# Performance work log

Hardware: AMD Instinct MI355X
Metric: run time of the kernel (lower is better)

Reference implementation:

```python
import jax, jax.numpy as jnp
import numpy as np

B, H, W, DIM = 4, 128, 128, 64
HEADS, DH, DR = 8, 64, 16
INNER = HEADS * DH  # 512
HID3 = 3 * DR       # 48, wavelet-MLP in_channels
HIDX = 2 * HID3     # 96, wavelet-MLP hidden


def _conv(x, w, stride=1, pad=0, groups=1):
    return jax.lax.conv_general_dilated(
        x, w, (stride, stride), [(pad, pad), (pad, pad)],
        dimension_numbers=('NCHW', 'OIHW', 'NCHW'), feature_group_count=groups)


def _gelu(x):
    return jax.nn.gelu(x, approximate=False)  # torch nn.GELU default (erf)


def _haar_kernel(C):
    h = np.array([[1., 1.], [1., 1.]]) / 2.
    g = np.array([[1., -1.], [1., -1.]]) / 2.
    ht = np.array([[1., 1.], [-1., -1.]]) / 2.
    gt = np.array([[1., -1.], [-1., 1.]]) / 2.
    k = np.stack([h, g, ht, gt])[:, None]          # [4,1,2,2]
    return jnp.asarray(np.tile(k, (C, 1, 1, 1)), jnp.float32)  # [4C,1,2,2], torch repeat layout


def _l2norm(x):
    return x / jnp.maximum(jnp.linalg.norm(x, axis=-1, keepdims=True), 1e-12)


def _spatial(x, dw, pw, gamma):  # SpitialUnit, x NHWC
    t = x.transpose(0, 3, 1, 2)
    C = t.shape[1]
    y = _conv(t, dw, pad=1, groups=C)
    y = _conv(_gelu(y), pw)
    return (t + gamma * y).transpose(0, 2, 3, 1)


def _fourier(x, al_pw, al_dw, ah_pw, ah_dw, ph_pw, ph_scale):  # FourierUnit, x NHWC
    t = x.transpose(0, 3, 1, 2)
    Bc, C, Hc, Wc = t.shape
    X = jnp.fft.rfft2(t, norm='ortho')
    amp, phase = jnp.abs(X), jnp.angle(X)
    Hf, Wf = amp.shape[-2], amp.shape[-1]
    yy = jnp.linspace(0., 1., Hf)[:, None]
    xx = jnp.linspace(0., 1., Wf)[None, :]
    rr = jnp.sqrt(yy ** 2 + xx ** 2)
    low = jax.nn.sigmoid((0.25 - rr) * 20.0)
    high = 1.0 - low
    a_lo = _conv(_gelu(_conv(amp * low[None, None], al_pw)), al_dw, pad=1, groups=C)
    a_hi = _conv(_gelu(_conv(amp * high[None, None], ah_pw)), ah_dw, pad=1, groups=C)
    amp_out = a_lo + a_hi
    phase_out = phase + ph_scale * _conv(phase, ph_pw)
    Y = jax.lax.complex(amp_out * jnp.cos(phase_out), amp_out * jnp.sin(phase_out))
    out = jnp.fft.irfft2(Y, s=(Hc, Wc), norm='ortho')
    return out.transpose(0, 2, 3, 1)


def _wavelet(x, bn_gamma, bn_beta, mlp_in, mlp_dw, mlp_out, res_scale):  # WaveletUnit, x NHWC (H,W even)
    t = x.transpose(0, 3, 1, 2)
    Bc, C, Hc, Wc = t.shape
    y = _conv(t, _haar_kernel(C), stride=2, groups=C)           # [B,4C,H/2,W/2]
    LL, LH, HL, HH = jnp.split(y, 4, axis=1)                    # torch chunk layout
    high = jnp.concatenate([LH, HL, HH], axis=1)                # [B,3C,H/2,W/2]
    # BatchNorm2d in eval mode: running_mean=0, running_var=1, eps=1e-5
    n = high * (bn_gamma / jnp.sqrt(1.0 + 1e-5))[None, :, None, None] + bn_beta[None, :, None, None]
    m = _conv(n, mlp_in)
    m = _gelu(_conv(m, mlp_dw, pad=1, groups=m.shape[1]))
    m = _conv(m, mlp_out)
    high_enh = high + res_scale * m
    x1, x2, x3 = jnp.split(high_enh, 3, axis=1)
    # IWT: out[..., 2i+p, 2j+q] = [LL, x1; x2, x3][p,q]
    arr = jnp.stack([jnp.stack([LL, x1], -1), jnp.stack([x2, x3], -1)], axis=-2)  # [B,C,h,w,p,q]
    Hh, Wh = LL.shape[-2], LL.shape[-1]
    out = arr.transpose(0, 1, 2, 4, 3, 5).reshape(Bc, C, Hh * 2, Wh * 2)
    return out.transpose(0, 2, 3, 1)


def reference(x_in, Wq, Wk, Wv, Wr, We, qs_dw, qs_pw, qs_gamma,
              al_pw, al_dw, ah_pw, ah_dw, ph_pw, ph_scale,
              bn_gamma, bn_beta, mlp_in, mlp_dw, mlp_out, res_scale,
              rescale, Wproj, bproj):
    b, h, w, c = x_in.shape
    hw = h * w
    heads = rescale.shape[0]
    dh = Wq.shape[1] // heads
    dr = Wr.shape[1]
    x = x_in.reshape(b, hw, c)
    q_inp, k_inp, v_inp = x @ Wq, x @ Wk, x @ Wv
    q_dim = (q_inp @ Wr).reshape(b, h, w, dr)
    k_dim = (k_inp @ Wr).reshape(b, h, w, dr)
    v_dim = (v_inp @ Wr).reshape(b, h, w, dr)
    q_mix = _spatial(q_dim, qs_dw, qs_pw, qs_gamma)
    k_mix = _fourier(k_dim, al_pw, al_dw, ah_pw, ah_dw, ph_pw, ph_scale)
    v_mix = _wavelet(v_dim, bn_gamma, bn_beta, mlp_in, mlp_dw, mlp_out, res_scale)
    q_new = q_mix.reshape(b, hw, dr) @ We
    k_new = k_mix.reshape(b, hw, dr) @ We
    v_new = v_mix.reshape(b, hw, dr) @ We

    def pack(t):  # -> [b, heads, dh, hw]
        return t.reshape(b, hw, heads, dh).transpose(0, 2, 3, 1)

    q, k, v = pack(q_new), pack(k_new), pack(v_new)
    q, k = _l2norm(q), _l2norm(k)                       # normalize over hw
    attn = jnp.einsum('bhdn,bhen->bhde', k, q)          # channel attention [b,H,dh,dh]
    attn = jax.nn.softmax(attn * rescale[None], axis=-1)
    o = jnp.einsum('bhde,bhen->bhdn', attn, v)          # [b,H,dh,hw]
    o = o.transpose(0, 3, 1, 2).reshape(b, hw, heads * dh)
    return (o @ Wproj + bproj).reshape(b, h, w, c)


def setup_inputs() -> dict:
    key = jax.random.key(0)
    ks = jax.random.split(key, 20)

    def nrm(k, shape, s=0.02):
        return jax.random.normal(k, shape, jnp.float32) * s

    return {
        'x_in': jax.random.normal(ks[0], (B, H, W, DIM), jnp.float32),
        'Wq': nrm(ks[1], (DIM, INNER)), 'Wk': nrm(ks[2], (DIM, INNER)), 'Wv': nrm(ks[3], (DIM, INNER)),
        'Wr': nrm(ks[4], (INNER, DR)), 'We': nrm(ks[5], (DR, INNER)),
        'qs_dw': nrm(ks[6], (DR, 1, 3, 3)), 'qs_pw': nrm(ks[7], (DR, DR, 1, 1)),
        'qs_gamma': jnp.zeros((1, DR, 1, 1), jnp.float32),
        'al_pw': nrm(ks[8], (DR, DR, 1, 1)), 'al_dw': nrm(ks[9], (DR, 1, 3, 3)),
        'ah_pw': nrm(ks[10], (DR, DR, 1, 1)), 'ah_dw': nrm(ks[11], (DR, 1, 3, 3)),
        'ph_pw': nrm(ks[12], (DR, DR, 1, 1)), 'ph_scale': jnp.asarray(0.01, jnp.float32),
        'bn_gamma': jnp.ones((HID3,), jnp.float32), 'bn_beta': jnp.zeros((HID3,), jnp.float32),
        'mlp_in': nrm(ks[13], (HIDX, HID3, 1, 1)), 'mlp_dw': nrm(ks[14], (HIDX, 1, 3, 3)),
        'mlp_out': nrm(ks[15], (HID3, HIDX, 1, 1)), 'res_scale': jnp.ones((1,), jnp.float32),
        'rescale': jnp.ones((HEADS, 1, 1), jnp.float32),
        'Wproj': nrm(ks[16], (INNER, DIM)), 'bproj': jnp.zeros((DIM,), jnp.float32),
    }
```

## Files before the change

kernel.cpp:

```cpp
#include <hip/hip_runtime.h>
#include <hip/hip_bf16.h>
#include <math.h>

#define HW 16384

__device__ __forceinline__ float LD(const void* p, long i, int bf){
  return bf ? __bfloat162float(((const __hip_bfloat16*)p)[i]) : ((const float*)p)[i];
}
__device__ __forceinline__ float geluf(float x){ return 0.5f*x*(1.0f + erff(x*0.70710678118654752f)); }
__device__ __forceinline__ int rev7(int i){ return (int)(__brev((unsigned)i)>>25); }

__device__ __forceinline__ void fft128(float* Ar, float* Ai, const float* ct, const float* st,
                                       int lane, float dir){
  #pragma unroll
  for(int len=2; len<=128; len<<=1){
    int half=len>>1;
    int pos = lane & (half-1);
    int i1 = ((lane & ~(half-1))<<1) | pos;
    int i2 = i1 + half;
    int tw = pos * (128/len);
    float wr = ct[tw], wi = dir*st[tw];
    float xr=Ar[i2], xi=Ai[i2];
    float tr = xr*wr - xi*wi;
    float ti = xr*wi + xi*wr;
    float ur=Ar[i1], ui=Ai[i1];
    Ar[i1]=ur+tr; Ai[i1]=ui+ti;
    Ar[i2]=ur-tr; Ai[i2]=ui-ti;
  }
}

#define MAKE_TWP(ct,st) { int tt=threadIdx.x; if(tt<128){ float ang=6.283185307179586f*(float)tt/128.f; float s_,c_; sincosf(ang,&s_,&c_); (ct)[tt]=c_; (st)[tt]=s_; } }

#define OFF_M    0
#define OFF_G    3072
#define OFF_MB   6144
#define OFF_FLAG 10240
#define OFF_QDIM 16384
#define OFF_KDIM (16384 + 1048576)
#define OFF_VDIM (16384 + 2*1048576)
#define OFF_QMIX (16384 + 3*1048576)
#define OFF_KMIX (16384 + 4*1048576)
#define OFF_S    (16384 + 5*1048576)
#define FSZ 532480

__global__ void k_head(const void* Wq, const void* Wk, const void* Wv,
                       const void* Wr, const void* bng, float* ws){
  __shared__ float wr[8192];
  __shared__ float part[256];
  int blk=blockIdx.x, t=threadIdx.x;
  if(blk==48){
    for(int i=3072+t;i<10240;i+=256) ws[i]=0.f;
    if(t==0){
      float v = ((const float*)bng)[0];
      ((int*)ws)[OFF_FLAG] = (v==1.0f) ? 0 : 1;
    }
    return;
  }
  int bf = (((const float*)bng)[0]==1.0f) ? 0 : 1;
  int mat=blk>>4, seg=blk&15;
  const void* Wsrc = mat==0 ? Wq : (mat==1 ? Wk : Wv);
  for(int i=t;i<8192;i+=256) wr[i]=LD(Wr,i,bf);
  __syncthreads();
  int o=t&63, jseg=t>>6;
  int c=seg*4+(o>>4), r=o&15;
  float acc=0.f;
  for(int j=jseg*128;j<jseg*128+128;j++) acc += LD(Wsrc,(long)c*512+j,bf)*wr[j*16+r];
  part[jseg*64+o]=acc;
  __syncthreads();
  if(t<64){
    float s=part[t]+part[64+t]+part[128+t]+part[192+t];
    int cc=seg*4+(t>>4), rr=t&15;
    ws[cc*48 + mat*16 + rr]=s;
  }
}

__global__ void k_dims(const void* x, const float* ws,
                       float* qd, float* kd, float* vd, const int* flg){
  int bf=*flg;
  __shared__ __align__(16) float ms[3072];
  __shared__ __align__(16) float xs[64*130];
  int t=threadIdx.x;
  int b = blockIdx.x>>7;
  int pix0 = (blockIdx.x&127)<<7;
  for(int i=t;i<3072;i+=256) ms[i]=ws[i];
  long base = ((long)b*HW + pix0)*64;
  if(!bf){
    const float4* xp = (const float4*)((const float*)x + base);
    for(int e=t;e<2048;e+=256){
      int px=e>>4, c4=(e&15)<<2;
      float4 v = xp[e];
      xs[(c4  )*130+px]=v.x; xs[(c4+1)*130+px]=v.y;
      xs[(c4+2)*130+px]=v.z; xs[(c4+3)*130+px]=v.w;
    }
  } else {
    const uint4* xp = (const uint4*)((const __hip_bfloat16*)x + base);
    for(int e=t;e<1024;e+=256){
// ... 129 lines not shown
    float* wiT=smem;
    float* vds=smem+4800;
    float* ns =smem+6848;
    float* gsm=smem+8416;
    float* bsm=smem+8464;
    int blk3=blk-512;
    int b = blk3>>7;
    int hpbase = (blk3&127)<<5;
    int i0 = hpbase>>6, j0 = hpbase&63;
    for(int i=t;i<4608;i+=256){ int ch=i/48, cc=i-ch*48; wiT[cc*100+ch]=LD(win,i,bf); }
    if(t<48){ gsm[t]=LD(bng,t,bf)*(1.f/sqrtf(1.f+1e-5f)); bsm[t]=LD(bnb,t,bf); }
    long rb0 = ((long)(b*128 + 2*i0)*128 + 2*j0)*16;
    {
      const float4* v4a=(const float4*)(vd+rb0);
      const float4* v4b=(const float4*)(vd+rb0+2048);
      ((float4*)vds)[t] = v4a[t];
      ((float4*)(vds+1024))[t] = v4b[t];
    }
    __syncthreads();
    for(int o=t;o<1536;o+=256){
      int p=o/48, cc=o-p*48;
      int m=cc+16, c=m>>2, f=m&3;
      float a =vds[(2*p)*16+c],      bv=vds[(2*p+1)*16+c];
      float cv=vds[1024+(2*p)*16+c], dvv=vds[1024+(2*p+1)*16+c];
      float v;
      if(f==0)      v=(a+bv+cv+dvv);
      else if(f==1) v=(a-bv+cv-dvv);
      else if(f==2) v=(a+bv-cv-dvv);
      else          v=(a-bv-cv+dvv);
      ns[p*49+cc] = v*0.5f*gsm[cc]+bsm[cc];
    }
    __syncthreads();
    int px=t>>3, chg=t&7;
    int ch0=chg*12;
    float4 a0={0,0,0,0}, a1={0,0,0,0}, a2={0,0,0,0};
    #pragma unroll 4
    for(int cc=0;cc<48;cc++){
      float nsv = ns[px*49+cc];
      const float4* wp = (const float4*)&wiT[cc*100+ch0];
      float4 w0=wp[0], w1=wp[1], w2=wp[2];
      a0.x+=nsv*w0.x; a0.y+=nsv*w0.y; a0.z+=nsv*w0.z; a0.w+=nsv*w0.w;
      a1.x+=nsv*w1.x; a1.y+=nsv*w1.y; a1.z+=nsv*w1.z; a1.w+=nsv*w1.w;
      a2.x+=nsv*w2.x; a2.y+=nsv*w2.y; a2.z+=nsv*w2.z; a2.w+=nsv*w2.w;
    }
    long ob = ((long)b*4096 + hpbase + px)*96 + ch0;
    float4* mp=(float4*)(m96+ob);
    mp[0]=a0; mp[1]=a1; mp[2]=a2;
  }
}

__global__ void k_fft_col(const float* Rre, const float* Rim,
                          float* glo, float* ghi, float* pho,
                          const void* alpw, const void* ahpw,
                          const void* phpw, const void* phs, const int* flg){
  __shared__ float sre[2080], sim[2080];
  __shared__ float og[2080], oh[2080], op[2080];
  __shared__ float Ar[512], Ai[512];
  __shared__ float ct[128], st[128];
  __shared__ float wl[256], wh[256], wp[256];
  int t=threadIdx.x;
  int bf=*flg;
  int b = blockIdx.x/65, v = blockIdx.x%65;
  MAKE_TWP(ct,st);
  wl[t]=LD(alpw,t,bf); wh[t]=LD(ahpw,t,bf); wp[t]=LD(phpw,t,bf);
  long ibase = ((long)b*128)*1040 + v*16;
  for(int e=t;e<2048;e+=256){
    int y=e>>4, c=e&15;
    sre[c*130+y]=Rre[ibase + (long)y*1040 + c];
    sim[c*130+y]=Rim[ibase + (long)y*1040 + c];
  }
  __syncthreads();
  int w=t>>6, l=t&63, wb=w<<7;
  const float inv=1.f/128.f;
  for(int c=w; c<16; c+=4){
    int sb=c*130;
    float x0r=sre[sb+l], x0i=sim[sb+l], x1r=sre[sb+64+l], x1i=sim[sb+64+l];
    int r0=rev7(l), r1=rev7(64+l);
    Ar[wb+r0]=x0r; Ai[wb+r0]=x0i;
    Ar[wb+r1]=x1r; Ai[wb+r1]=x1i;
    fft128(Ar+wb, Ai+wb, ct, st, l, -1.f);
    float re0=Ar[wb+l]*inv, im0=Ai[wb+l]*inv;
    float re1=Ar[wb+64+l]*inv, im1=Ai[wb+64+l]*inv;
    sre[sb+l]=sqrtf(re0*re0+im0*im0); sim[sb+l]=atan2f(im0,re0);
    sre[sb+64+l]=sqrtf(re1*re1+im1*im1); sim[sb+64+l]=atan2f(im1,re1);
  }
  __syncthreads();
  {
    int u = t&127, half = t>>7;
    float yy=(float)u/127.f, xx=(float)v/64.f;
    float rr=sqrtf(yy*yy+xx*xx);
    float lo = 1.f/(1.f+expf((rr-0.25f)*20.f));
    float hi = 1.f-lo;
    float av[16], pv[16];
    for(int ch=0;ch<16;ch++){ av[ch]=sre[ch*130+u]; pv[ch]=sim[ch*130+u]; }
    float pscale = LD(phs,0,bf);
    for(int c=half*8;c<half*8+8;c++){
      float al=0.f, ah=0.f, pp=0.f;
      for(int ch=0;ch<16;ch++){
        float a=av[ch];
        al += wl[c*16+ch]*(a*lo);
        ah += wh[c*16+ch]*(a*hi);
        pp += wp[c*16+ch]*pv[ch];
      }
      og[c*130+u]=geluf(al); oh[c*130+u]=geluf(ah); op[c*130+u]=pv[c]+pscale*pp;
    }
  }
  __syncthreads();
  long obase = ((long)b*128)*1040 + v*16;
  for(int e=t;e<2048;e+=256){
    int u=e>>4, c=e&15;
    long o = obase + (long)u*1040 + c;
    glo[o]=og[c*130+u]; ghi[o]=oh[c*130+u]; pho[o]=op[c*130+u];
  }
}

__global__ void k_four_dw(const float* glo, const float* ghi, const float* pho,
                          float* Yre, float* Yim,
                          const void* aldw, const void* ahdw, const int* flg){
  int bf=*flg;
  __shared__ float wl[144], wh[144];
  int t=threadIdx.x;
  if(t<144){wl[t]=LD(aldw,t,bf); wh[t]=LD(ahdw,t,bf);}
  __syncthreads();
  long o = (long)blockIdx.x*256+t;
  int c=(int)(o&15); long r=o>>4; int v=(int)(r%65); long r2=r/65; int u=(int)(r2&127); int b=(int)(r2>>7);
  float acc=0.f;
  for(int dp=0;dp<3;dp++){
    int uu=u-1+dp; if(uu<0||uu>=128) continue;
    for(int dq=0;dq<3;dq++){
      int vv=v-1+dq; if(vv<0||vv>=65) continue;
      long idx=(((long)(b*128+uu))*65+vv)*16+c;
      acc += wl[c*9+dp*3+dq]*glo[idx] + wh[c*9+dp*3+dq]*ghi[idx];
    }
  }
  float pvv = pho[o];
  float s_,c_; sincosf(pvv,&s_,&c_);
  Yre[o]=acc*c_; Yim[o]=acc*s_;
}

__global__ void k_ifft_col(const float* Yre, const float* Yim, float* Zre, float* Zim){
  __shared__ float sre[2080], sim[2080];
  __shared__ float Ar[512], Ai[512];
  __shared__ float ct[128], st[128];
  int t=threadIdx.x;
  int b = blockIdx.x/65, v = blockIdx.x%65;
  MAKE_TWP(ct,st);
  long ibase = ((long)b*128)*1040 + v*16;
  for(int e=t;e<2048;e+=256){
    int u=e>>4, c=e&15;
    sre[c*130+u]=Yre[ibase + (long)u*1040 + c];
    sim[c*130+u]=Yim[ibase + (long)u*1040 + c];
  }
  __syncthreads();
  int w=t>>6, l=t&63, wb=w<<7;
  for(int c=w; c<16; c+=4){
    int sb=c*130;
    float x0r=sre[sb+l], x0i=sim[sb+l], x1r=sre[sb+64+l], x1i=sim[sb+64+l];
    int r0=rev7(l), r1=rev7(64+l);
    Ar[wb+r0]=x0r; Ai[wb+r0]=x0i;
    Ar[wb+r1]=x1r; Ai[wb+r1]=x1i;
    fft128(Ar+wb, Ai+wb, ct, st, l, +1.f);
    sre[sb+l]=Ar[wb+l]; sim[sb+l]=Ai[wb+l];
    sre[sb+64+l]=Ar[wb+64+l]; sim[sb+64+l]=Ai[wb+64+l];
  }
  __syncthreads();
  for(int e=t;e<2048;e+=256){
    int y=e>>4, c=e&15;
    Zre[ibase + (long)y*1040 + c]=sre[c*130+y];
    Zim[ibase + (long)y*1040 + c]=sim[c*130+y];
  }
}

__global__ void k_mix2(const float* Zre, const float* Zim, const float* qm,
                       const float* m96, float* g96, const void* wdw_,
                       float* G, const int* flg){
  __shared__ float smem[9664];
  int blk=blockIdx.x, t=threadIdx.x;
  if(blk<256){
    float* szre=smem; float* szim=smem+2112; float* oslab=smem+4224;
    float* Ar=smem+8384; float* Ai=smem+8896; float* ct=smem+9408; float* st=smem+9536;
    int b = blk>>6, y0 = (blk&63)<<1;
    MAKE_TWP(ct,st);
    long ibase = ((long)(b*128+y0))*1040;
    for(int e=t;e<2080;e+=256){
      int yl=e/1040, rem=e%1040, v=rem>>4, c=rem&15;
      szre[yl*1056 + c*66 + v]=Zre[ibase+e];
      szim[yl*1056 + c*66 + v]=Zim[ibase+e];
    }
    __syncthreads();
    int w=t>>6, l=t&63, wb=w<<7;
    const float inv=1.f/128.f;
    for(int li=w; li<32; li+=4){
      int yl=li>>4, c=li&15;
      int sb = yl*1056 + c*66;
      float zr0 = szre[sb+l];
      float zi0 = (l==0)?0.f:szim[sb+l];
      float zr1, zi1;
      if(l==0){ zr1=szre[sb+64]; zi1=0.f; }
      else    { zr1=szre[sb+64-l]; zi1=-szim[sb+64-l]; }
      int r0=rev7(l), r1=rev7(64+l);
      Ar[wb+r0]=zr0; Ai[wb+r0]=zi0;
      Ar[wb+r1]=zr1; Ai[wb+r1]=zi1;
      fft128(Ar+wb, Ai+wb, ct, st, l, +1.f);
      int ob = yl*2080 + c*130;
      oslab[ob+l]=Ar[wb+l]*inv;
      oslab[ob+64+l]=Ar[wb+64+l]*inv;
    }
    __syncthreads();
    float* qs = smem;
    long qbase = ((long)(b*128+y0))*2048;
    for(int e=t;e<4096;e+=256) qs[e]=qm[qbase+e];
    __syncthreads();
    int r=t>>4, s=t&15;
    float akq=0.f, akk=0.f, aqq=0.f;
    for(int p=0;p<256;p++){
      int yl=p>>7, x=p&127;
      float kr = oslab[yl*2080 + r*130 + x];
      float ks_ = oslab[yl*2080 + s*130 + x];
      float qr = qs[p*16+r];
      float qsv= qs[p*16+s];
      akq += kr*qsv;
      akk += kr*ks_;
      aqq += qr*qsv;
    }
    float* Gb=G + b*768;
    atomicAdd(&Gb[t], akq);
    atomicAdd(&Gb[256+t], akk);
    atomicAdd(&Gb[512+t], aqq);
  } else {
    int bf=*flg;
    float* wdw=smem;
    for(int i=t;i<864;i+=256) wdw[i]=LD(wdw_,i,bf);
    __syncthreads();
    int o = (blk-256)*256+t;
    int ch = o%96; int r = o/96; int px = r&4095; int b = r>>12;
    int i = px>>6, j = px&63;
    long mb = (long)b*393216;
    float acc=0.f;
    for(int dp=0;dp<3;dp++){ int ii=i-1+dp; if(ii<0||ii>=64) continue;
      for(int dq=0;dq<3;dq++){ int jj=j-1+dq; if(jj<0||jj>=64) continue;
        acc += wdw[ch*9+dp*3+dq]*m96[mb + (long)(ii*64+jj)*96 + ch]; } }
    g96[o]=geluf(acc);
  }
}

__global__ void k_attn(const float* G, float* Mb, const void* We,
                       const void* Wproj, const void* resc, const int* flg){
  int bf=*flg;
  __shared__ float wes[16*64];
  __shared__ float gkq[256], gkk[256], gqq[256];
  __shared__ float ukq[64*16], ukk[64*16], uqq[64*16];
  __shared__ float nk[64], nq[64];
  __shared__ float A[64*64];
  __shared__ float T[64*16];
  __shared__ float wpj[64*64];
  int b=blockIdx.x>>3, h=blockIdx.x&7;
  int t=threadIdx.x;
  for(int i=t;i<1024;i+=256){ int rr=i>>6, e=i&63; wes[rr*64+e]=LD(We, (long)rr*512 + h*64 + e, bf); }
  gkq[t]=G[b*768+t]; gkk[t]=G[b*768+256+t]; gqq[t]=G[b*768+512+t];
  for(int i=t;i<4096;i+=256){ int d=i>>6, c=i&63; wpj[i]=LD(Wproj,(long)(h*64+d)*64+c,bf); }
  __syncthreads();
  for(int i=t;i<1024;i+=256){
    int d=i>>4, s=i&15;
    float a1=0.f,a2=0.f,a3=0.f;
    for(int rr=0;rr<16;rr++){ float wv=wes[rr*64+d]; a1+=wv*gkq[rr*16+s]; a2+=wv*gkk[rr*16+s]; a3+=wv*gqq[rr*16+s]; }
    ukq[i]=a1; ukk[i]=a2; uqq[i]=a3;
  }
  __syncthreads();
  if(t<64){ float a=0.f; for(int s=0;s<16;s++) a+=ukk[t*16+s]*wes[s*64+t]; nk[t]=fmaxf(sqrtf(a),1e-12f); }
  else if(t<128){ int e=t-64; float a=0.f; for(int s=0;s<16;s++) a+=uqq[e*16+s]*wes[s*64+e]; nq[e]=fmaxf(sqrtf(a),1e-12f); }
  __syncthreads();
  float rsc=LD(resc,h,bf);
  for(int i=t;i<4096;i+=256){
    int d=i>>6, e=i&63;
    float a=0.f; for(int s=0;s<16;s++) a+=ukq[d*16+s]*wes[s*64+e];
    A[i]=a/(nk[d]*nq[e])*rsc;
  }
  __syncthreads();
  if(t<64){
    int d=t; float m=-1e30f;
    for(int e=0;e<64;e++) m=fmaxf(m,A[d*64+e]);
    float sum=0.f;
    for(int e=0;e<64;e++){ float ev=expf(A[d*64+e]-m); A[d*64+e]=ev; sum+=ev; }
    float inv=1.f/sum;
    for(int e=0;e<64;e++) A[d*64+e]*=inv;
  }
  __syncthreads();
  for(int i=t;i<1024;i+=256){
    int d=i>>4, s=i&15;
    float a=0.f; for(int e=0;e<64;e++) a+=A[d*64+e]*wes[s*64+e];
    T[i]=a;
  }
  __syncthreads();
  for(int i=t;i<1024;i+=256){
    int s=i>>6, c=i&63;
    float a=0.f; for(int d=0;d<64;d++) a+=T[d*16+s]*wpj[d*64+c];
    atomicAdd(&Mb[b*1024 + s*64 + c], a);
  }
}

__global__ void k_epi2(const float* g96, const float* vd, const float* Mb_,
                       const void* wout_, const void* rs_, const void* bproj,
                       void* out, const int* flg){
  int bf=*flg;
  __shared__ __align__(16) float sg[32*104];
  __shared__ __align__(16) float swt[48*100];
  __shared__ __align__(16) float smb[1024];
  __shared__ float sbias[64];
  int t=threadIdx.x;
  int b = blockIdx.x>>7;
  int rem = blockIdx.x&127;
  int gi = rem>>1;
  int gj0 = (rem&1)<<5;

  long gb = ((long)b*4096 + gi*64 + gj0)*96;
  for(int e=t;e<3072;e+=256){ int px=e/96, ch=e-px*96; sg[px*104+ch]=g96[gb+e]; }
  for(int e=t;e<4608;e+=256){ int cc=e/96, ch=e-cc*96; swt[cc*100+ch]=LD(wout_, e, bf); }
  for(int i=t;i<1024;i+=256) smb[i]=Mb_[b*1024+i];
  if(t<64) sbias[t]=LD(bproj,t,bf);
  __syncthreads();

  int tpx=t>>4, tcc=t&15;
  int px0=tpx<<1, cc0=tcc*3;
  float a00=0.f,a01=0.f,a02=0.f,a10=0.f,a11=0.f,a12=0.f;
  const float4* g4=(const float4*)sg;
  const float4* w4=(const float4*)swt;
  #pragma unroll 4
  for(int ch4=0; ch4<24; ch4++){
    float4 ga=g4[px0*26+ch4], gbv=g4[(px0+1)*26+ch4];
    float4 w0=w4[cc0*25+ch4], w1=w4[(cc0+1)*25+ch4], w2=w4[(cc0+2)*25+ch4];
    a00 += ga.x*w0.x+ga.y*w0.y+ga.z*w0.z+ga.w*w0.w;
    a01 += ga.x*w1.x+ga.y*w1.y+ga.z*w1.z+ga.w*w1.w;
    a02 += ga.x*w2.x+ga.y*w2.y+ga.z*w2.z+ga.w*w2.w;
    a10 += gbv.x*w0.x+gbv.y*w0.y+gbv.z*w0.z+gbv.w*w0.w;
    a11 += gbv.x*w1.x+gbv.y*w1.y+gbv.z*w1.z+gbv.w*w1.w;
    a12 += gbv.x*w2.x+gbv.y*w2.y+gbv.z*w2.z+gbv.w*w2.w;
  }
  __syncthreads();

  float* she = sg;
  float rs=LD(rs_,0,bf);
  float accv[2][3]={{a00,a01,a02},{a10,a11,a12}};
  #pragma unroll
  for(int i=0;i<2;i++)
    #pragma unroll
    for(int j=0;j<3;j++){
      int pxl=px0+i, cc=cc0+j, gj=gj0+pxl;
      int m=cc+16, c=m>>2, f=m&3;
      long vb=((long)(b*128+2*gi)*128 + 2*gj)*16;
      float a=vd[vb+c], bv=vd[vb+16+c], cv=vd[vb+2048+c], dv=vd[vb+2064+c];
      float hv;
      if(f==0)      hv=(a+bv+cv+dv);
      else if(f==1) hv=(a-bv+cv-dv);
      else if(f==2) hv=(a+bv-cv-dv);
      else          hv=(a-bv-cv+dv);
      she[pxl*64 + 16 + cc] = hv*0.5f + rs*accv[i][j];
    }
  for(int o=t;o<512;o+=256){
    int pxl=o>>4, c16=o&15, gj=gj0+pxl;
    int c=c16>>2, f=c16&3;
    long vb=((long)(b*128+2*gi)*128 + 2*gj)*16;
    float a=vd[vb+c], bv=vd[vb+16+c], cv=vd[vb+2048+c], dv=vd[vb+2064+c];
    float hv;
    if(f==0)      hv=(a+bv+cv+dv);
    else if(f==1) hv=(a-bv+cv-dv);
    else if(f==2) hv=(a+bv-cv-dv);
    else          hv=(a-bv-cv+dv);
    she[pxl*64 + c16] = hv*0.5f;
  }
  __syncthreads();

  int c=t&63, xg=t>>6;
  float mbr[16];
  #pragma unroll
  for(int s=0;s<16;s++) mbr[s]=smb[s*64+c];
  float bb=sbias[c];
  long ob0 = ((long)(b*128+2*gi)*128 + 2*gj0)*64;
  for(int k=0;k<32;k++){
    int o=xg+(k<<2);
    int r=o>>6, xl=o&63;
    int hp=xl>>1, pos=((r&1)<<1)|(xl&1);
    const float4* h4=(const float4*)(she + hp*64 + pos*16);
    float4 h0=h4[0],h1=h4[1],h2=h4[2],h3=h4[3];
    float acc=bb;
    acc += h0.x*mbr[0]+h0.y*mbr[1]+h0.z*mbr[2]+h0.w*mbr[3];
    acc += h1.x*mbr[4]+h1.y*mbr[5]+h1.z*mbr[6]+h1.w*mbr[7];
    acc += h2.x*mbr[8]+h2.y*mbr[9]+h2.z*mbr[10]+h2.w*mbr[11];
    acc += h3.x*mbr[12]+h3.y*mbr[13]+h3.z*mbr[14]+h3.w*mbr[15];
    long oo = ob0 + (long)r*8192 + (long)xl*64 + c;
    if(bf) ((__hip_bfloat16*)out)[oo]=__float2bfloat16(acc);
    else   ((float*)out)[oo]=acc;
  }
}

extern "C" void kernel_launch(void* const* d_in, const int* in_sizes, int n_in,
                              void* d_out, int out_size, void* d_ws, size_t ws_size,
                              hipStream_t stream) {
  const void* x_in   = d_in[0];
  const void* Wq     = d_in[1];
  const void* Wk     = d_in[2];
  const void* Wv     = d_in[3];
  const void* Wr     = d_in[4];
  const void* We     = d_in[5];
  const void* qs_dw  = d_in[6];
  const void* qs_pw  = d_in[7];
  const void* qs_g   = d_in[8];
  const void* al_pw  = d_in[9];
  const void* al_dw  = d_in[10];
  const void* ah_pw  = d_in[11];
  const void* ah_dw  = d_in[12];
  const void* ph_pw  = d_in[13];
  const void* ph_s   = d_in[14];
  const void* bn_g   = d_in[15];
  const void* bn_b   = d_in[16];
  const void* mlp_in = d_in[17];
  const void* mlp_dw = d_in[18];
  const void* mlp_out= d_in[19];
  const void* res_s  = d_in[20];
  const void* rescale= d_in[21];
  const void* Wproj  = d_in[22];
  const void* bproj  = d_in[23];
  float* ws = (float*)d_ws;
  const int* flg = ((const int*)ws) + OFF_FLAG;

  float* FA = ws + OFF_S;
  float* FB = FA + FSZ;
  float* FC = FB + FSZ;
  float* FD = FC + FSZ;
  float* FE = FD + FSZ;
  float* M96 = FE + FSZ;
  float* G96 = ws + OFF_QDIM;

  k_head<<<49,256,0,stream>>>(Wq,Wk,Wv,Wr,bn_g, ws);
  k_dims<<<512,256,0,stream>>>(x_in, ws, ws+OFF_QDIM, ws+OFF_KDIM, ws+OFF_VDIM, flg);
  k_mix3<<<1024,256,0,stream>>>(ws+OFF_QDIM, ws+OFF_QMIX, qs_dw, qs_pw, qs_g,
                                ws+OFF_KDIM, FA, FB,
                                ws+OFF_VDIM, M96, mlp_in, bn_g, bn_b, flg);
  k_fft_col<<<260,256,0,stream>>>(FA, FB, FC, FD, FE, al_pw, ah_pw, ph_pw, ph_s, flg);
  k_four_dw<<<2080,256,0,stream>>>(FC, FD, FE, FA, FB, al_dw, ah_dw, flg);
  k_ifft_col<<<260,256,0,stream>>>(FA, FB, FC, FD);
  k_mix2<<<6400,256,0,stream>>>(FC, FD, ws+OFF_QMIX, M96, G96, mlp_dw, ws+OFF_G, flg);
  k_attn<<<32,256,0,stream>>>(ws+OFF_G, ws+OFF_MB, We, Wproj, rescale, flg);
  k_epi2<<<512,256,0,stream>>>(G96, ws+OFF_VDIM, ws+OFF_MB, mlp_out, res_s, bproj, d_out, flg);
}
```

Baseline: 271.0 us.

## Fuse Fourier depthwise conv into inverse column FFT and spread wavelet dwconv

The Fourier amplitude depthwise conv and phase recombination are folded into the inverse column FFT kernel, which now loads three neighbouring frequency columns into shared memory. This removes one launch and an intermediate round trip through global memory. The wavelet MLP depthwise conv blocks, previously attached to the row-IFFT/Gram kernel, are split across the two column-FFT launches so that the 260 FFT blocks run alongside otherwise idle capacity. In exchange, each fused block carries a larger shared-memory footprint and reads three columns of redundant input.

```diff
diff --git a/kernel.cpp b/kernel.cpp
--- a/kernel.cpp
+++ b/kernel.cpp
@@ -42,6 +42,17 @@
 #define OFF_KMIX (16384 + 4*1048576)
 #define OFF_S    (16384 + 5*1048576)
 #define FSZ 532480
+
+__device__ __forceinline__ void wave_dw_body(int o, const float* m96, float* g96, const float* wdw){
+  int ch = o%96; int r = o/96; int px = r&4095; int b = r>>12;
+  int i = px>>6, j = px&63;
+  long mb = (long)b*393216;
+  float acc=0.f;
+  for(int dp=0;dp<3;dp++){ int ii=i-1+dp; if(ii<0||ii>=64) continue;
+    for(int dq=0;dq<3;dq++){ int jj=j-1+dq; if(jj<0||jj>=64) continue;
+      acc += wdw[ch*9+dp*3+dq]*m96[mb + (long)(ii*64+jj)*96 + ch]; } }
+  g96[o]=geluf(acc);
+}
 
 __global__ void k_head(const void* Wq, const void* Wk, const void* Wv,
                        const void* Wr, const void* bng, float* ws){
@@ -277,7 +288,9 @@
 __global__ void k_fft_col(const float* Rre, const float* Rim,
                           float* glo, float* ghi, float* pho,
                           const void* alpw, const void* ahpw,
-                          const void* phpw, const void* phs, const int* flg){
+                          const void* phpw, const void* phs,
+                          const float* m96, float* g96, const void* wdw_,
+                          const int* flg){
   __shared__ float sre[2080], sim[2080];
   __shared__ float og[2080], oh[2080], op[2080];
   __shared__ float Ar[512], Ai[512];
@@ -285,7 +298,15 @@
   __shared__ float wl[256], wh[256], wp[256];
   int t=threadIdx.x;
   int bf=*flg;
-  int b = blockIdx.x/65, v = blockIdx.x%65;
+  int blk=blockIdx.x;
+  if(blk>=260){
+    float* wdw=sre;
+    for(int i=t;i<864;i+=256) wdw[i]=LD(wdw_,i,bf);
+    __syncthreads();
+    wave_dw_body((blk-260)*256+t, m96, g96, wdw);
+    return;
+  }
+  int b = blk/65, v = blk%65;
   MAKE_TWP(ct,st);
   wl[t]=LD(alpw,t,bf); wh[t]=LD(ahpw,t,bf); wp[t]=LD(phpw,t,bf);
   long ibase = ((long)b*128)*1040 + v*16;
@@ -339,42 +360,67 @@
   }
 }
 
-__global__ void k_four_dw(const float* glo, const float* ghi, const float* pho,
-                          float* Yre, float* Yim,
-                          const void* aldw, const void* ahdw, const int* flg){
+__global__ void k_ifft_four(const float* glo, const float* ghi, const float* pho,
+                            float* Zre, float* Zim,
+                            const void* aldw, const void* ahdw,
+                            const float* m96, float* g96, const void* wdw_,
+                            const int* flg){
+  __shared__ float smem[20064];
+  int t=threadIdx.x;
+  int blk=blockIdx.x;
   int bf=*flg;
-  __shared__ float wl[144], wh[144];
-  int t=threadIdx.x;
-  if(t<144){wl[t]=LD(aldw,t,bf); wh[t]=LD(ahdw,t,bf);}
-  __syncthreads();
-  long o = (long)blockIdx.x*256+t;
-  int c=(int)(o&15); long r=o>>4; int v=(int)(r%65); long r2=r/65; int u=(int)(r2&127); int b=(int)(r2>>7);
-  float acc=0.f;
-  for(int dp=0;dp<3;dp++){
-    int uu=u-1+dp; if(uu<0||uu>=128) continue;
-    for(int dq=0;dq<3;dq++){
-      int vv=v-1+dq; if(vv<0||vv>=65) continue;
-      long idx=(((long)(b*128+uu))*65+vv)*16+c;
-      acc += wl[c*9+dp*3+dq]*glo[idx] + wh[c*9+dp*3+dq]*ghi[idx];
-    }
-  }
-  float pvv = pho[o];
-  float s_,c_; sincosf(pvv,&s_,&c_);
-  Yre[o]=acc*c_; Yim[o]=acc*s_;
-}
-
-__global__ void k_ifft_col(const float* Yre, const float* Yim, float* Zre, float* Zim){
-  __shared__ float sre[2080], sim[2080];
-  __shared__ float Ar[512], Ai[512];
-  __shared__ float ct[128], st[128];
-  int t=threadIdx.x;
-  int b = blockIdx.x/65, v = blockIdx.x%65;
+  if(blk>=260){
+    float* wdw=smem;
+    for(int i=t;i<864;i+=256) wdw[i]=LD(wdw_,i,bf);
+    __syncthreads();
+    wave_dw_body((blk-260+3072)*256+t, m96, g96, wdw);
+    return;
+  }
+  float* g3 =smem;
+  float* h3 =smem+6144;
+  float* ph =smem+12288;
+  float* sre=smem+14336;
+  float* sim=smem+16416;
+  float* Ar =smem+18496;
+  float* Ai =smem+19008;
+  float* ct =smem+19520;
+  float* st =smem+19648;
+  float* wl =smem+19776;
+  float* wh =smem+19920;
+  int b = blk/65, v = blk%65;
   MAKE_TWP(ct,st);
-  long ibase = ((long)b*128)*1040 + v*16;
+  if(t<144){ wl[t]=LD(aldw,t,bf); wh[t]=LD(ahdw,t,bf); }
+  for(int col=0;col<3;col++){
+    int vv=v-1+col;
+    long ib = ((long)b*128)*1040 + (long)vv*16;
+    if(vv>=0 && vv<65){
+      for(int e=t;e<2048;e+=256){
+        int u=e>>4, c=e&15;
+        g3[col*2048+e]=glo[ib+(long)u*1040+c];
+        h3[col*2048+e]=ghi[ib+(long)u*1040+c];
+      }
+    } else {
+      for(int e=t;e<2048;e+=256){ g3[col*2048+e]=0.f; h3[col*2048+e]=0.f; }
+    }
+  }
+  {
+    long ib = ((long)b*128)*1040 + (long)v*16;
+    for(int e=t;e<2048;e+=256){ int u=e>>4, c=e&15; ph[e]=pho[ib+(long)u*1040+c]; }
+  }
+  __syncthreads();
   for(int e=t;e<2048;e+=256){
     int u=e>>4, c=e&15;
-    sre[c*130+u]=Yre[ibase + (long)u*1040 + c];
-    sim[c*130+u]=Yim[ibase + (long)u*1040 + c];
+    float acc=0.f;
+    #pragma unroll
+    for(int dp=0;dp<3;dp++){
+      int uu=u-1+dp; if(uu<0||uu>=128) continue;
+      int rowb=uu*16+c;
+      acc += wl[c*9+dp*3  ]*g3[rowb]      + wh[c*9+dp*3  ]*h3[rowb];
+      acc += wl[c*9+dp*3+1]*g3[2048+rowb] + wh[c*9+dp*3+1]*h3[2048+rowb];
+      acc += wl[c*9+dp*3+2]*g3[4096+rowb] + wh[c*9+dp*3+2]*h3[4096+rowb];
+    }
+    float s_,c_; sincosf(ph[e],&s_,&c_);
+    sre[c*130+u]=acc*c_; sim[c*130+u]=acc*s_;
   }
   __syncthreads();
   int w=t>>6, l=t&63, wb=w<<7;
@@ -389,6 +435,7 @@
     sre[sb+64+l]=Ar[wb+64+l]; sim[sb+64+l]=Ai[wb+64+l];
   }
   __syncthreads();
+  long ibase = ((long)b*128)*1040 + v*16;
   for(int e=t;e<2048;e+=256){
     int y=e>>4, c=e&15;
     Zre[ibase + (long)y*1040 + c]=sre[c*130+y];
@@ -396,77 +443,60 @@
   }
 }
 
-__global__ void k_mix2(const float* Zre, const float* Zim, const float* qm,
-                       const float* m96, float* g96, const void* wdw_,
-                       float* G, const int* flg){
+__global__ void k_irow_gram(const float* Zre, const float* Zim, const float* qm,
+                            float* G, const int* flg){
   __shared__ float smem[9664];
   int blk=blockIdx.x, t=threadIdx.x;
-  if(blk<256){
-    float* szre=smem; float* szim=smem+2112; float* oslab=smem+4224;
-    float* Ar=smem+8384; float* Ai=smem+8896; float* ct=smem+9408; float* st=smem+9536;
-    int b = blk>>6, y0 = (blk&63)<<1;
-    MAKE_TWP(ct,st);
-    long ibase = ((long)(b*128+y0))*1040;
-    for(int e=t;e<2080;e+=256){
-      int yl=e/1040, rem=e%1040, v=rem>>4, c=rem&15;
-      szre[yl*1056 + c*66 + v]=Zre[ibase+e];
-      szim[yl*1056 + c*66 + v]=Zim[ibase+e];
-    }
-    __syncthreads();
-    int w=t>>6, l=t&63, wb=w<<7;
-    const float inv=1.f/128.f;
-    for(int li=w; li<32; li+=4){
-      int yl=li>>4, c=li&15;
-      int sb = yl*1056 + c*66;
-      float zr0 = szre[sb+l];
-      float zi0 = (l==0)?0.f:szim[sb+l];
-      float zr1, zi1;
-      if(l==0){ zr1=szre[sb+64]; zi1=0.f; }
-      else    { zr1=szre[sb+64-l]; zi1=-szim[sb+64-l]; }
-      int r0=rev7(l), r1=rev7(64+l);
-      Ar[wb+r0]=zr0; Ai[wb+r0]=zi0;
-      Ar[wb+r1]=zr1; Ai[wb+r1]=zi1;
-      fft128(Ar+wb, Ai+wb, ct, st, l, +1.f);
-      int ob = yl*2080 + c*130;
-      oslab[ob+l]=Ar[wb+l]*inv;
-      oslab[ob+64+l]=Ar[wb+64+l]*inv;
-    }
-    __syncthreads();
-    float* qs = smem;
-    long qbase = ((long)(b*128+y0))*2048;
-    for(int e=t;e<4096;e+=256) qs[e]=qm[qbase+e];
-    __syncthreads();
-    int r=t>>4, s=t&15;
-    float akq=0.f, akk=0.f, aqq=0.f;
-    for(int p=0;p<256;p++){
-      int yl=p>>7, x=p&127;
-      float kr = oslab[yl*2080 + r*130 + x];
-      float ks_ = oslab[yl*2080 + s*130 + x];
-      float qr = qs[p*16+r];
-      float qsv= qs[p*16+s];
-      akq += kr*qsv;
-      akk += kr*ks_;
-      aqq += qr*qsv;
-    }
-    float* Gb=G + b*768;
-    atomicAdd(&Gb[t], akq);
-    atomicAdd(&Gb[256+t], akk);
-    atomicAdd(&Gb[512+t], aqq);
-  } else {
-    int bf=*flg;
-    float* wdw=smem;
-    for(int i=t;i<864;i+=256) wdw[i]=LD(wdw_,i,bf);
-    __syncthreads();
-    int o = (blk-256)*256+t;
-    int ch = o%96; int r = o/96; int px = r&4095; int b = r>>12;
-    int i = px>>6, j = px&63;
-    long mb = (long)b*393216;
-    float acc=0.f;
-    for(int dp=0;dp<3;dp++){ int ii=i-1+dp; if(ii<0||ii>=64) continue;
-      for(int dq=0;dq<3;dq++){ int jj=j-1+dq; if(jj<0||jj>=64) continue;
-        acc += wdw[ch*9+dp*3+dq]*m96[mb + (long)(ii*64+jj)*96 + ch]; } }
-    g96[o]=geluf(acc);
-  }
+  float* szre=smem; float* szim=smem+2112; float* oslab=smem+4224;
+  float* Ar=smem+8384; float* Ai=smem+8896; float* ct=smem+9408; float* st=smem+9536;
+  int b = blk>>6, y0 = (blk&63)<<1;
+  MAKE_TWP(ct,st);
+  long ibase = ((long)(b*128+y0))*1040;
+  for(int e=t;e<2080;e+=256){
+    int yl=e/1040, rem=e%1040, v=rem>>4, c=rem&15;
+    szre[yl*1056 + c*66 + v]=Zre[ibase+e];
+    szim[yl*1056 + c*66 + v]=Zim[ibase+e];
+  }
+  __syncthreads();
+  int w=t>>6, l=t&63, wb=w<<7;
+  const float inv=1.f/128.f;
+  for(int li=w; li<32; li+=4){
+    int yl=li>>4, c=li&15;
+    int sb = yl*1056 + c*66;
+    float zr0 = szre[sb+l];
+    float zi0 = (l==0)?0.f:szim[sb+l];
+    float zr1, zi1;
+    if(l==0){ zr1=szre[sb+64]; zi1=0.f; }
+    else    { zr1=szre[sb+64-l]; zi1=-szim[sb+64-l]; }
+    int r0=rev7(l), r1=rev7(64+l);
+    Ar[wb+r0]=zr0; Ai[wb+r0]=zi0;
+    Ar[wb+r1]=zr1; Ai[wb+r1]=zi1;
+    fft128(Ar+wb, Ai+wb, ct, st, l, +1.f);
+    int ob = yl*2080 + c*130;
+    oslab[ob+l]=Ar[wb+l]*inv;
+    oslab[ob+64+l]=Ar[wb+64+l]*inv;
+  }
+  __syncthreads();
+  float* qs = smem;
+  long qbase = ((long)(b*128+y0))*2048;
+  for(int e=t;e<4096;e+=256) qs[e]=qm[qbase+e];
+  __syncthreads();
+  int r=t>>4, s=t&15;
+  float akq=0.f, akk=0.f, aqq=0.f;
+  for(int p=0;p<256;p++){
+    int yl=p>>7, x=p&127;
+    float kr = oslab[yl*2080 + r*130 + x];
+    float ks_ = oslab[yl*2080 + s*130 + x];
+    float qr = qs[p*16+r];
+    float qsv= qs[p*16+s];
+    akq += kr*qsv;
+    akk += kr*ks_;
+    aqq += qr*qsv;
+  }
+  float* Gb=G + b*768;
+  atomicAdd(&Gb[t], akq);
+  atomicAdd(&Gb[256+t], akk);
+  atomicAdd(&Gb[512+t], aqq);
 }
 
 __global__ void k_attn(const float* G, float* Mb, const void* We,
@@ -661,10 +691,11 @@
   k_mix3<<<1024,256,0,stream>>>(ws+OFF_QDIM, ws+OFF_QMIX, qs_dw, qs_pw, qs_g,
                                 ws+OFF_KDIM, FA, FB,
                                 ws+OFF_VDIM, M96, mlp_in, bn_g, bn_b, flg);
-  k_fft_col<<<260,256,0,stream>>>(FA, FB, FC, FD, FE, al_pw, ah_pw, ph_pw, ph_s, flg);
-  k_four_dw<<<2080,256,0,stream>>>(FC, FD, FE, FA, FB, al_dw, ah_dw, flg);
-  k_ifft_col<<<260,256,0,stream>>>(FA, FB, FC, FD);
-  k_mix2<<<6400,256,0,stream>>>(FC, FD, ws+OFF_QMIX, M96, G96, mlp_dw, ws+OFF_G, flg);
+  k_fft_col<<<3332,256,0,stream>>>(FA, FB, FC, FD, FE, al_pw, ah_pw, ph_pw, ph_s,
+                                   M96, G96, mlp_dw, flg);
+  k_ifft_four<<<3332,256,0,stream>>>(FC, FD, FE, FA, FB, al_dw, ah_dw,
+                                     M96, G96, mlp_dw, flg);
+  k_irow_gram<<<256,256,0,stream>>>(FA, FB, ws+OFF_QMIX, ws+OFF_G, flg);
   k_attn<<<32,256,0,stream>>>(ws+OFF_G, ws+OFF_MB, We, Wproj, rescale, flg);
   k_epi2<<<512,256,0,stream>>>(G96, ws+OFF_VDIM, ws+OFF_MB, mlp_out, res_s, bproj, d_out, flg);
 }
```

After: 279.5 us. 1.03x slower.

## Spread wavelet depthwise conv across FFT kernels and halve epilogue tile size

Applied to the files above, without the earlier changes.

The wavelet MLP depthwise 3x3 conv + GELU (6144 blocks) was appended to the row-iFFT/Gram kernel. It is now split into three chunks of 2048 blocks, placed as extra blocks in the column FFT, column iFFT and row-iFFT/Gram kernels. Those FFT kernels launch only 260 or 256 blocks, so the extra independent work fills otherwise idle CUs. Separately, the epilogue kernel now handles 16 pixels per block instead of 32, doubling the grid for more parallelism, at the cost of reloading the weights per block more often.

```diff
diff --git a/kernel.cpp b/kernel.cpp
--- a/kernel.cpp
+++ b/kernel.cpp
@@ -42,6 +42,17 @@
 #define OFF_KMIX (16384 + 4*1048576)
 #define OFF_S    (16384 + 5*1048576)
 #define FSZ 532480
+
+__device__ __forceinline__ void wave_dw_body(int o, const float* m96, float* g96, const float* wdw){
+  int ch = o%96; int r = o/96; int px = r&4095; int b = r>>12;
+  int i = px>>6, j = px&63;
+  long mb = (long)b*393216;
+  float acc=0.f;
+  for(int dp=0;dp<3;dp++){ int ii=i-1+dp; if(ii<0||ii>=64) continue;
+    for(int dq=0;dq<3;dq++){ int jj=j-1+dq; if(jj<0||jj>=64) continue;
+      acc += wdw[ch*9+dp*3+dq]*m96[mb + (long)(ii*64+jj)*96 + ch]; } }
+  g96[o]=geluf(acc);
+}
 
 __global__ void k_head(const void* Wq, const void* Wk, const void* Wv,
                        const void* Wr, const void* bng, float* ws){
@@ -277,7 +288,9 @@
 __global__ void k_fft_col(const float* Rre, const float* Rim,
                           float* glo, float* ghi, float* pho,
                           const void* alpw, const void* ahpw,
-                          const void* phpw, const void* phs, const int* flg){
+                          const void* phpw, const void* phs,
+                          const float* m96, float* g96, const void* wdw_,
+                          const int* flg){
   __shared__ float sre[2080], sim[2080];
   __shared__ float og[2080], oh[2080], op[2080];
   __shared__ float Ar[512], Ai[512];
@@ -285,7 +298,15 @@
   __shared__ float wl[256], wh[256], wp[256];
   int t=threadIdx.x;
   int bf=*flg;
-  int b = blockIdx.x/65, v = blockIdx.x%65;
+  int blk=blockIdx.x;
+  if(blk>=260){
+    float* wdw=sre;
+    for(int i=t;i<864;i+=256) wdw[i]=LD(wdw_,i,bf);
+    __syncthreads();
+    wave_dw_body((blk-260)*256+t, m96, g96, wdw);
+    return;
+  }
+  int b = blk/65, v = blk%65;
   MAKE_TWP(ct,st);
   wl[t]=LD(alpw,t,bf); wh[t]=LD(ahpw,t,bf); wp[t]=LD(phpw,t,bf);
   long ibase = ((long)b*128)*1040 + v*16;
@@ -363,12 +384,22 @@
   Yre[o]=acc*c_; Yim[o]=acc*s_;
 }
 
-__global__ void k_ifft_col(const float* Yre, const float* Yim, float* Zre, float* Zim){
+__global__ void k_ifft_col(const float* Yre, const float* Yim, float* Zre, float* Zim,
+                           const float* m96, float* g96, const void* wdw_, const int* flg){
   __shared__ float sre[2080], sim[2080];
   __shared__ float Ar[512], Ai[512];
   __shared__ float ct[128], st[128];
   int t=threadIdx.x;
-  int b = blockIdx.x/65, v = blockIdx.x%65;
+  int blk=blockIdx.x;
+  if(blk>=260){
+    int bf=*flg;
+    float* wdw=sre;
+    for(int i=t;i<864;i+=256) wdw[i]=LD(wdw_,i,bf);
+    __syncthreads();
+    wave_dw_body((blk-260+2048)*256+t, m96, g96, wdw);
+    return;
+  }
+  int b = blk/65, v = blk%65;
   MAKE_TWP(ct,st);
   long ibase = ((long)b*128)*1040 + v*16;
   for(int e=t;e<2048;e+=256){
@@ -396,77 +427,69 @@
   }
 }
 
-__global__ void k_mix2(const float* Zre, const float* Zim, const float* qm,
-                       const float* m96, float* g96, const void* wdw_,
-                       float* G, const int* flg){
+__global__ void k_irow_gram(const float* Zre, const float* Zim, const float* qm,
+                            float* G, const float* m96, float* g96, const void* wdw_,
+                            const int* flg){
   __shared__ float smem[9664];
   int blk=blockIdx.x, t=threadIdx.x;
-  if(blk<256){
-    float* szre=smem; float* szim=smem+2112; float* oslab=smem+4224;
-    float* Ar=smem+8384; float* Ai=smem+8896; float* ct=smem+9408; float* st=smem+9536;
-    int b = blk>>6, y0 = (blk&63)<<1;
-    MAKE_TWP(ct,st);
-    long ibase = ((long)(b*128+y0))*1040;
-    for(int e=t;e<2080;e+=256){
-      int yl=e/1040, rem=e%1040, v=rem>>4, c=rem&15;
-      szre[yl*1056 + c*66 + v]=Zre[ibase+e];
-      szim[yl*1056 + c*66 + v]=Zim[ibase+e];
-    }
-    __syncthreads();
-    int w=t>>6, l=t&63, wb=w<<7;
-    const float inv=1.f/128.f;
-    for(int li=w; li<32; li+=4){
-      int yl=li>>4, c=li&15;
-      int sb = yl*1056 + c*66;
-      float zr0 = szre[sb+l];
-      float zi0 = (l==0)?0.f:szim[sb+l];
-      float zr1, zi1;
-      if(l==0){ zr1=szre[sb+64]; zi1=0.f; }
-      else    { zr1=szre[sb+64-l]; zi1=-szim[sb+64-l]; }
-      int r0=rev7(l), r1=rev7(64+l);
-      Ar[wb+r0]=zr0; Ai[wb+r0]=zi0;
-      Ar[wb+r1]=zr1; Ai[wb+r1]=zi1;
-      fft128(Ar+wb, Ai+wb, ct, st, l, +1.f);
-      int ob = yl*2080 + c*130;
-      oslab[ob+l]=Ar[wb+l]*inv;
-      oslab[ob+64+l]=Ar[wb+64+l]*inv;
-    }
-    __syncthreads();
-    float* qs = smem;
-    long qbase = ((long)(b*128+y0))*2048;
-    for(int e=t;e<4096;e+=256) qs[e]=qm[qbase+e];
-    __syncthreads();
-    int r=t>>4, s=t&15;
-    float akq=0.f, akk=0.f, aqq=0.f;
-    for(int p=0;p<256;p++){
-      int yl=p>>7, x=p&127;
-      float kr = oslab[yl*2080 + r*130 + x];
-      float ks_ = oslab[yl*2080 + s*130 + x];
-      float qr = qs[p*16+r];
-      float qsv= qs[p*16+s];
-      akq += kr*qsv;
-      akk += kr*ks_;
-      aqq += qr*qsv;
-    }
-    float* Gb=G + b*768;
-    atomicAdd(&Gb[t], akq);
-    atomicAdd(&Gb[256+t], akk);
-    atomicAdd(&Gb[512+t], aqq);
-  } else {
+  if(blk>=256){
     int bf=*flg;
     float* wdw=smem;
     for(int i=t;i<864;i+=256) wdw[i]=LD(wdw_,i,bf);
     __syncthreads();
-    int o = (blk-256)*256+t;
-    int ch = o%96; int r = o/96; int px = r&4095; int b = r>>12;
-    int i = px>>6, j = px&63;
-    long mb = (long)b*393216;
-    float acc=0.f;
-    for(int dp=0;dp<3;dp++){ int ii=i-1+dp; if(ii<0||ii>=64) continue;
-      for(int dq=0;dq<3;dq++){ int jj=j-1+dq; if(jj<0||jj>=64) continue;
-        acc += wdw[ch*9+dp*3+dq]*m96[mb + (long)(ii*64+jj)*96 + ch]; } }
-    g96[o]=geluf(acc);
-  }
+    wave_dw_body((blk-256+4096)*256+t, m96, g96, wdw);
+    return;
+  }
+  float* szre=smem; float* szim=smem+2112; float* oslab=smem+4224;
+  float* Ar=smem+8384; float* Ai=smem+8896; float* ct=smem+9408; float* st=smem+9536;
+  int b = blk>>6, y0 = (blk&63)<<1;
+  MAKE_TWP(ct,st);
+  long ibase = ((long)(b*128+y0))*1040;
+  for(int e=t;e<2080;e+=256){
+    int yl=e/1040, rem=e%1040, v=rem>>4, c=rem&15;
+    szre[yl*1056 + c*66 + v]=Zre[ibase+e];
+    szim[yl*1056 + c*66 + v]=Zim[ibase+e];
+  }
+  __syncthreads();
+  int w=t>>6, l=t&63, wb=w<<7;
+  const float inv=1.f/128.f;
+  for(int li=w; li<32; li+=4){
+    int yl=li>>4, c=li&15;
+    int sb = yl*1056 + c*66;
+    float zr0 = szre[sb+l];
+    float zi0 = (l==0)?0.f:szim[sb+l];
+    float zr1, zi1;
+    if(l==0){ zr1=szre[sb+64]; zi1=0.f; }
+    else    { zr1=szre[sb+64-l]; zi1=-szim[sb+64-l]; }
+    int r0=rev7(l), r1=rev7(64+l);
+    Ar[wb+r0]=zr0; Ai[wb+r0]=zi0;
+    Ar[wb+r1]=zr1; Ai[wb+r1]=zi1;
+    fft128(Ar+wb, Ai+wb, ct, st, l, +1.f);
+    int ob = yl*2080 + c*130;
+    oslab[ob+l]=Ar[wb+l]*inv;
+    oslab[ob+64+l]=Ar[wb+64+l]*inv;
+  }
+  __syncthreads();
+  float* qs = smem;
+  long qbase = ((long)(b*128+y0))*2048;
+  for(int e=t;e<4096;e+=256) qs[e]=qm[qbase+e];
+  __syncthreads();
+  int r=t>>4, s=t&15;
+  float akq=0.f, akk=0.f, aqq=0.f;
+  for(int p=0;p<256;p++){
+    int yl=p>>7, x=p&127;
+    float kr = oslab[yl*2080 + r*130 + x];
+    float ks_ = oslab[yl*2080 + s*130 + x];
+    float qr = qs[p*16+r];
+    float qsv= qs[p*16+s];
+    akq += kr*qsv;
+    akk += kr*ks_;
+    aqq += qr*qsv;
+  }
+  float* Gb=G + b*768;
+  atomicAdd(&Gb[t], akq);
+  atomicAdd(&Gb[256+t], akk);
+  atomicAdd(&Gb[512+t], aqq);
 }
 
 __global__ void k_attn(const float* G, float* Mb, const void* We,
@@ -528,70 +551,65 @@
                        const void* wout_, const void* rs_, const void* bproj,
                        void* out, const int* flg){
   int bf=*flg;
-  __shared__ __align__(16) float sg[32*104];
+  __shared__ __align__(16) float sg[16*104];
   __shared__ __align__(16) float swt[48*100];
   __shared__ __align__(16) float smb[1024];
   __shared__ float sbias[64];
   int t=threadIdx.x;
-  int b = blockIdx.x>>7;
-  int rem = blockIdx.x&127;
-  int gi = rem>>1;
-  int gj0 = (rem&1)<<5;
+  int b = blockIdx.x>>8;
+  int rem = blockIdx.x&255;
+  int gi = rem>>2;
+  int gj0 = (rem&3)<<4;
 
   long gb = ((long)b*4096 + gi*64 + gj0)*96;
-  for(int e=t;e<3072;e+=256){ int px=e/96, ch=e-px*96; sg[px*104+ch]=g96[gb+e]; }
+  for(int e=t;e<1536;e+=256){ int px=e/96, ch=e-px*96; sg[px*104+ch]=g96[gb+e]; }
   for(int e=t;e<4608;e+=256){ int cc=e/96, ch=e-cc*96; swt[cc*100+ch]=LD(wout_, e, bf); }
   for(int i=t;i<1024;i+=256) smb[i]=Mb_[b*1024+i];
   if(t<64) sbias[t]=LD(bproj,t,bf);
   __syncthreads();
 
-  int tpx=t>>4, tcc=t&15;
-  int px0=tpx<<1, cc0=tcc*3;
-  float a00=0.f,a01=0.f,a02=0.f,a10=0.f,a11=0.f,a12=0.f;
+  int px=t>>4, ccg=t&15;
+  int cc0=ccg*3;
+  float a0=0.f,a1=0.f,a2=0.f;
   const float4* g4=(const float4*)sg;
   const float4* w4=(const float4*)swt;
   #pragma unroll 4
   for(int ch4=0; ch4<24; ch4++){
-    float4 ga=g4[px0*26+ch4], gbv=g4[(px0+1)*26+ch4];
+    float4 ga=g4[px*26+ch4];
     float4 w0=w4[cc0*25+ch4], w1=w4[(cc0+1)*25+ch4], w2=w4[(cc0+2)*25+ch4];
-    a00 += ga.x*w0.x+ga.y*w0.y+ga.z*w0.z+ga.w*w0.w;
-    a01 += ga.x*w1.x+ga.y*w1.y+ga.z*w1.z+ga.w*w1.w;
-    a02 += ga.x*w2.x+ga.y*w2.y+ga.z*w2.z+ga.w*w2.w;
-    a10 += gbv.x*w0.x+gbv.y*w0.y+gbv.z*w0.z+gbv.w*w0.w;
-    a11 += gbv.x*w1.x+gbv.y*w1.y+gbv.z*w1.z+gbv.w*w1.w;
-    a12 += gbv.x*w2.x+gbv.y*w2.y+gbv.z*w2.z+gbv.w*w2.w;
+    a0 += ga.x*w0.x+ga.y*w0.y+ga.z*w0.z+ga.w*w0.w;
+    a1 += ga.x*w1.x+ga.y*w1.y+ga.z*w1.z+ga.w*w1.w;
+    a2 += ga.x*w2.x+ga.y*w2.y+ga.z*w2.z+ga.w*w2.w;
   }
   __syncthreads();
 
   float* she = sg;
   float rs=LD(rs_,0,bf);
-  float accv[2][3]={{a00,a01,a02},{a10,a11,a12}};
+  float accv[3]={a0,a1,a2};
+  int gj=gj0+px;
+  long vb=((long)(b*128+2*gi)*128 + 2*gj)*16;
   #pragma unroll
-  for(int i=0;i<2;i++)
-    #pragma unroll
-    for(int j=0;j<3;j++){
-      int pxl=px0+i, cc=cc0+j, gj=gj0+pxl;
-      int m=cc+16, c=m>>2, f=m&3;
-      long vb=((long)(b*128+2*gi)*128 + 2*gj)*16;
-      float a=vd[vb+c], bv=vd[vb+16+c], cv=vd[vb+2048+c], dv=vd[vb+2064+c];
-      float hv;
-      if(f==0)      hv=(a+bv+cv+dv);
-      else if(f==1) hv=(a-bv+cv-dv);
-      else if(f==2) hv=(a+bv-cv-dv);
-      else          hv=(a-bv-cv+dv);
-      she[pxl*64 + 16 + cc] = hv*0.5f + rs*accv[i][j];
-    }
-  for(int o=t;o<512;o+=256){
-    int pxl=o>>4, c16=o&15, gj=gj0+pxl;
-    int c=c16>>2, f=c16&3;
-    long vb=((long)(b*128+2*gi)*128 + 2*gj)*16;
+  for(int j=0;j<3;j++){
+    int cc=cc0+j;
+    int m=cc+16, c=m>>2, f=m&3;
     float a=vd[vb+c], bv=vd[vb+16+c], cv=vd[vb+2048+c], dv=vd[vb+2064+c];
     float hv;
     if(f==0)      hv=(a+bv+cv+dv);
     else if(f==1) hv=(a-bv+cv-dv);
     else if(f==2) hv=(a+bv-cv-dv);
     else          hv=(a-bv-cv+dv);
-    she[pxl*64 + c16] = hv*0.5f;
+    she[px*64 + 16 + cc] = hv*0.5f + rs*accv[j];
+  }
+  {
+    int c16=ccg;
+    int c=c16>>2, f=c16&3;
+    float a=vd[vb+c], bv=vd[vb+16+c], cv=vd[vb+2048+c], dv=vd[vb+2064+c];
+    float hv;
+    if(f==0)      hv=(a+bv+cv+dv);
+    else if(f==1) hv=(a-bv+cv-dv);
+    else if(f==2) hv=(a+bv-cv-dv);
+    else          hv=(a-bv-cv+dv);
+    she[px*64 + c16] = hv*0.5f;
   }
   __syncthreads();
 
@@ -601,9 +619,9 @@
   for(int s=0;s<16;s++) mbr[s]=smb[s*64+c];
   float bb=sbias[c];
   long ob0 = ((long)(b*128+2*gi)*128 + 2*gj0)*64;
-  for(int k=0;k<32;k++){
+  for(int k=0;k<16;k++){
     int o=xg+(k<<2);
-    int r=o>>6, xl=o&63;
+    int r=o>>5, xl=o&31;
     int hp=xl>>1, pos=((r&1)<<1)|(xl&1);
     const float4* h4=(const float4*)(she + hp*64 + pos*16);
     float4 h0=h4[0],h1=h4[1],h2=h4[2],h3=h4[3];
@@ -661,10 +679,11 @@
   k_mix3<<<1024,256,0,stream>>>(ws+OFF_QDIM, ws+OFF_QMIX, qs_dw, qs_pw, qs_g,
                                 ws+OFF_KDIM, FA, FB,
                                 ws+OFF_VDIM, M96, mlp_in, bn_g, bn_b, flg);
-  k_fft_col<<<260,256,0,stream>>>(FA, FB, FC, FD, FE, al_pw, ah_pw, ph_pw, ph_s, flg);
+  k_fft_col<<<2308,256,0,stream>>>(FA, FB, FC, FD, FE, al_pw, ah_pw, ph_pw, ph_s,
+                                   M96, G96, mlp_dw, flg);
   k_four_dw<<<2080,256,0,stream>>>(FC, FD, FE, FA, FB, al_dw, ah_dw, flg);
-  k_ifft_col<<<260,256,0,stream>>>(FA, FB, FC, FD);
-  k_mix2<<<6400,256,0,stream>>>(FC, FD, ws+OFF_QMIX, M96, G96, mlp_dw, ws+OFF_G, flg);
+  k_ifft_col<<<2308,256,0,stream>>>(FA, FB, FC, FD, M96, G96, mlp_dw, flg);
+  k_irow_gram<<<2304,256,0,stream>>>(FC, FD, ws+OFF_QMIX, ws+OFF_G, M96, G96, mlp_dw, flg);
   k_attn<<<32,256,0,stream>>>(ws+OFF_G, ws+OFF_MB, We, Wproj, rescale, flg);
-  k_epi2<<<512,256,0,stream>>>(G96, ws+OFF_VDIM, ws+OFF_MB, mlp_out, res_s, bproj, d_out, flg);
-}
+  k_epi2<<<1024,256,0,stream>>>(G96, ws+OFF_VDIM, ws+OFF_MB, mlp_out, res_s, bproj, d_out, flg);
+}
```

Result: no change. 267.6 us (-1.3%).
